# Kernel tuning notes

Measured on AMD Instinct MI355X. Metric: run time of the kernel, lower is better.

Reference implementation:

```python
import jax, jax.numpy as jnp
import numpy as np
import math

D_MODEL = 1024
N_HEADS = 16
D_K = D_MODEL // N_HEADS
D_FF = 4096
B, S = 4, 2048
EPS = 1e-5


def layer_norm(x, scale, bias):
    mu = jnp.mean(x, axis=-1, keepdims=True)
    var = jnp.mean(jnp.square(x - mu), axis=-1, keepdims=True)
    return (x - mu) * jax.lax.rsqrt(var + EPS) * scale + bias


def setup_inputs() -> dict:
    key = jax.random.key(0)
    ks = jax.random.split(key, 16)
    init = lambda k, shape, fan_in: jax.random.normal(k, shape, jnp.float32) / np.sqrt(fan_in)
    x = jax.random.normal(ks[0], (B, S, D_MODEL), jnp.float32)
    # causal mask: positions where mask==0 are blocked
    mask = jnp.tril(jnp.ones((S, S), dtype=bool))[None, None, :, :]
    return {
        "x": x,
        "mask": mask,
        "wq": init(ks[1], (D_MODEL, D_MODEL), D_MODEL), "bq": jnp.zeros((D_MODEL,), jnp.float32),
        "wk": init(ks[2], (D_MODEL, D_MODEL), D_MODEL), "bk": jnp.zeros((D_MODEL,), jnp.float32),
        "wv": init(ks[3], (D_MODEL, D_MODEL), D_MODEL), "bv": jnp.zeros((D_MODEL,), jnp.float32),
        "wo": init(ks[4], (D_MODEL, D_MODEL), D_MODEL), "bo": jnp.zeros((D_MODEL,), jnp.float32),
        "w1": init(ks[5], (D_FF, D_MODEL), D_MODEL), "b1": jnp.zeros((D_FF,), jnp.float32),
        "w2": init(ks[6], (D_MODEL, D_FF), D_FF), "b2": jnp.zeros((D_MODEL,), jnp.float32),
        "ln1_s": jnp.ones((D_MODEL,), jnp.float32), "ln1_b": jnp.zeros((D_MODEL,), jnp.float32),
        "ln2_s": jnp.ones((D_MODEL,), jnp.float32), "ln2_b": jnp.zeros((D_MODEL,), jnp.float32),
    }


def reference(x, mask, wq, bq, wk, bk, wv, bv, wo, bo, w1, b1, w2, b2, ln1_s, ln1_b, ln2_s, ln2_b):
    b, s, _ = x.shape
    # projections (torch Linear: y = x @ W.T + b); split heads -> [b, h, s, d_k]
    def proj(w, bias):
        return (jnp.einsum('bsd,ed->bse', x, w) + bias).reshape(b, s, N_HEADS, D_K).transpose(0, 2, 1, 3)
    Q, K, V = proj(wq, bq), proj(wk, bk), proj(wv, bv)
    scores = jnp.einsum('bhqd,bhkd->bhqk', Q, K) / math.sqrt(D_K)  # [b,h,s,s]
    scores = jnp.where(mask, scores, jnp.float32(-1e9))
    attn = jax.nn.softmax(scores, axis=-1)
    ctx = jnp.einsum('bhqk,bhkd->bhqd', attn, V)
    ctx = ctx.transpose(0, 2, 1, 3).reshape(b, s, D_MODEL)
    attn_out = jnp.einsum('bsd,ed->bse', ctx, wo) + bo
    h = layer_norm(x + attn_out, ln1_s, ln1_b)
    ff = jnp.einsum('bsd,fd->bsf', h, w1) + b1
    ff = jax.nn.gelu(ff, approximate=False)
    ff = jnp.einsum('bsf,df->bsd', ff, w2) + b2
    return layer_norm(h + ff, ln2_s, ln2_b)
```

## Files before the change

kernel.cpp:

```cpp
#include <hip/hip_runtime.h>
#include <hip/hip_bf16.h>
#include <math.h>

using bf16 = __hip_bfloat16;
using bf16x8 = __attribute__((ext_vector_type(8))) short;
using f32x4 = __attribute__((ext_vector_type(4))) float;

#define D_MODEL 1024
#define N_HEADS 16
#define D_K 64
#define D_FF 4096
#define BATCH 4
#define SEQ 2048
#define M_TOT (BATCH*SEQ)

__device__ __forceinline__ void async_copy16(void* lds, const void* g) {
    __builtin_amdgcn_global_load_lds((const __attribute__((address_space(1))) void*)g,
                                     (__attribute__((address_space(3))) void*)lds, 16, 0, 0);
}

__global__ void __launch_bounds__(256) cvt_kernel(const float* __restrict__ src,
                                                  bf16* __restrict__ dst, int n) {
    int nchunk = n >> 2;
    int stride = gridDim.x * blockDim.x;
    for (int i = blockIdx.x * blockDim.x + threadIdx.x; i < nchunk; i += stride) {
        float4 v = *(const float4*)&src[i * 4];
        union { bf16 h[4]; short4 s; } u;
        u.h[0] = __float2bfloat16(v.x);
        u.h[1] = __float2bfloat16(v.y);
        u.h[2] = __float2bfloat16(v.z);
        u.h[3] = __float2bfloat16(v.w);
        *(short4*)&dst[i * 4] = u.s;
    }
}

template<int EPI>
__global__ void __launch_bounds__(256) gemm_bt(const bf16* __restrict__ A,
                                               const bf16* __restrict__ B,
                                               const float* __restrict__ bias,
                                               const float* __restrict__ resid,
                                               float* __restrict__ Cf,
                                               bf16* __restrict__ Cb,
                                               int M, int N, int K) {
    __shared__ __align__(16) bf16 As[128 * 32];
    __shared__ __align__(16) bf16 Bs[128 * 32];
    const int tid  = threadIdx.x;
    const int lane = tid & 63;
    const int wave = tid >> 6;
    const int quad = lane >> 4;
    const int l16  = lane & 15;
    const int wr   = (wave >> 1) * 64;
    const int wc   = (wave & 1) * 64;
    const int m0   = blockIdx.y * 128;
    const int n0   = blockIdx.x * 128;

    const bf16* Ag = A + (size_t)m0 * K;
    const bf16* Bg = B + (size_t)n0 * K;

    f32x4 acc[4][4] = {};

    for (int k0 = 0; k0 < K; k0 += 32) {
        __syncthreads();
#pragma unroll
        for (int p = 0; p < 2; p++) {
            int c = p * 256 + tid;
            int row = c >> 2;
            int col = (c & 3) << 3;
            async_copy16(&As[c * 8], Ag + (size_t)row * K + k0 + col);
            async_copy16(&Bs[c * 8], Bg + (size_t)row * K + k0 + col);
        }
        __syncthreads();
        bf16x8 a[4], b[4];
#pragma unroll
        for (int i = 0; i < 4; i++)
            a[i] = *(const bf16x8*)&As[(wr + i * 16 + l16) * 32 + quad * 8];
#pragma unroll
        for (int j = 0; j < 4; j++)
            b[j] = *(const bf16x8*)&Bs[(wc + j * 16 + l16) * 32 + quad * 8];
#pragma unroll
        for (int i = 0; i < 4; i++)
#pragma unroll
            for (int j = 0; j < 4; j++)
                acc[i][j] = __builtin_amdgcn_mfma_f32_16x16x32_bf16(a[i], b[j], acc[i][j], 0, 0, 0);
    }

#pragma unroll
    for (int i = 0; i < 4; i++) {
#pragma unroll
        for (int r = 0; r < 4; r++) {
            int row = m0 + wr + i * 16 + quad * 4 + r;
            size_t rb = (size_t)row * N;
#pragma unroll
            for (int j = 0; j < 4; j++) {
                int col = n0 + wc + j * 16 + l16;
                float v = acc[i][j][r] + bias[col];
                if (EPI == 0) {
                    Cb[rb + col] = __float2bfloat16(v);
                } else if (EPI == 1) {
                    Cf[rb + col] = v + resid[rb + col];
                } else if (EPI == 2) {
                    float g = 0.5f * v * (1.0f + erff(v * 0.70710678118654752f));
                    Cb[rb + col] = __float2bfloat16(g);
                } else {
                    float sc = (col < 1024) ? 0.18033688011112043f : 1.0f;
                    Cb[rb + col] = __float2bfloat16(v * sc);
                }
            }
        }
    }
}

__global__ void __launch_bounds__(256) attn_kernel(const bf16* __restrict__ qkv,
                                                   bf16* __restrict__ ctx) {
    const int pair = blockIdx.x;
    const int h    = blockIdx.y;
    const int bb   = blockIdx.z;
    const int tid  = threadIdx.x;
    const int lane = tid & 63;
    const int wave = tid >> 6;
    const int quad = lane >> 4;
    const int l16  = lane & 15;

    __shared__ __align__(16) bf16 Pool[4 * 32 * 80];
    __shared__ __align__(16) bf16 Ks[2][64 * 64];
    __shared__ __align__(16) bf16 Vt[2][64 * 80];

    const size_t rowbase = (size_t)(bb * SEQ) * 3072;
    bf16* Pw = &Pool[wave * 32 * 80];
    const int swkey = (l16 >> 2) & 3;

#pragma unroll 1
    for (int phase = 0; phase < 2; phase++) {
        const int qb = (phase == 0) ? pair : (15 - pair);
        const int q0 = qb * 128;
        const int nkb = 2 * (qb + 1);

        __syncthreads();

#pragma unroll
        for (int p = 0; p < 4; p++) {
            int c = p * 256 + tid;
            int row = c >> 3;
            int off = (c & 7) * 8;
            async_copy16(&Pool[c * 8], qkv + rowbase + (size_t)(q0 + row) * 3072 + h * 64 + off);
        }
#pragma unroll
        for (int p = 0; p < 2; p++) {
            int c = p * 256 + tid;
            async_copy16(&Ks[0][c * 8],
                         qkv + rowbase + (size_t)(c >> 3) * 3072 + 1024 + h * 64 + (c & 7) * 8);
        }
        const int vk  = tid & 63;
        const int vd0a = (tid >> 6) * 8;
        const int vd0b = vd0a + 32;
        bf16x8 vr0 = *(const bf16x8*)&qkv[rowbase + (size_t)vk * 3072 + 2048 + h * 64 + vd0a];
        bf16x8 vr1 = *(const bf16x8*)&qkv[rowbase + (size_t)vk * 3072 + 2048 + h * 64 + vd0b];

        __syncthreads();

        bf16x8 aq[2][2];
#pragma unroll
        for (int i = 0; i < 2; i++)
#pragma unroll
            for (int kd = 0; kd < 2; kd++)
                aq[i][kd] = *(const bf16x8*)&Pool[(wave * 32 + i * 16 + l16) * 64 + kd * 32 + quad * 8];

#pragma unroll
        for (int u = 0; u < 8; u++) {
            Vt[0][(vd0a + u) * 80 + vk] = ((const bf16*)&vr0)[u];
            Vt[0][(vd0b + u) * 80 + vk] = ((const bf16*)&vr1)[u];
        }

        f32x4 o[2][4] = {};
        float l_acc[2][4] = {};

#pragma unroll 1
        for (int kb = 0; kb < nkb; kb++) {
            const int cur = kb & 1;
            const int nxt = cur ^ 1;
            __syncthreads();

            const bool pf = (kb + 1 < nkb);
            bf16x8 nv0, nv1;
            if (pf) {
#pragma unroll
                for (int p = 0; p < 2; p++) {
                    int c = p * 256 + tid;
                    async_copy16(&Ks[nxt][c * 8],
                                 qkv + rowbase + (size_t)((kb + 1) * 64 + (c >> 3)) * 3072 + 1024 + h * 64 + (c & 7) * 8);
                }
                nv0 = *(const bf16x8*)&qkv[rowbase + (size_t)((kb + 1) * 64 + vk) * 3072 + 2048 + h * 64 + vd0a];
                nv1 = *(const bf16x8*)&qkv[rowbase + (size_t)((kb + 1) * 64 + vk) * 3072 + 2048 + h * 64 + vd0b];
            }

            f32x4 s[2][4] = {};
#pragma unroll
            for (int jb = 0; jb < 4; jb++) {
#pragma unroll
                for (int kd = 0; kd < 2; kd++) {
                    bf16x8 bk = *(const bf16x8*)&Ks[cur][(jb * 16 + l16) * 64 + kd * 32 + quad * 8];
#pragma unroll
                    for (int i = 0; i < 2; i++)
                        s[i][jb] = __builtin_amdgcn_mfma_f32_16x16x32_bf16(aq[i][kd], bk, s[i][jb], 0, 0, 0);
                }
            }

            if (pf) {
#pragma unroll
                for (int u = 0; u < 8; u++) {
                    Vt[nxt][(vd0a + u) * 80 + vk] = ((const bf16*)&nv0)[u];
                    Vt[nxt][(vd0b + u) * 80 + vk] = ((const bf16*)&nv1)[u];
                }
            }

            const bool diagb = (kb >= 2 * qb);
#pragma unroll
            for (int i = 0; i < 2; i++) {
                const int row0 = q0 + wave * 32 + i * 16;
                const bool needmask = diagb && (kb * 64 + 63 > row0);
#pragma unroll
                for (int jb = 0; jb < 4; jb++) {
                    const int colg = kb * 64 + jb * 16 + l16;
                    const int colsw = ((jb ^ quad) * 16) + l16;
#pragma unroll
                    for (int r = 0; r < 4; r++) {
                        float t = s[i][jb][r];
                        if (needmask && colg > row0 + quad * 4 + r) t = -1e30f;
                        float p = exp2f(t);
                        l_acc[i][r] += p;
                        Pw[(i * 16 + quad * 4 + r) * 80 + colsw] = __float2bfloat16(p);
                    }
                }
            }

#pragma unroll
            for (int kk = 0; kk < 2; kk++) {
                bf16x8 bv[4];
#pragma unroll
                for (int nb = 0; nb < 4; nb++)
                    bv[nb] = *(const bf16x8*)&Vt[cur][(nb * 16 + l16) * 80 + kk * 32 + quad * 8];
                const int grp = kk * 2 + (quad >> 1);
                const int coff = ((grp ^ swkey) * 16) + (quad & 1) * 8;
#pragma unroll
                for (int i = 0; i < 2; i++) {
                    bf16x8 ap = *(const bf16x8*)&Pw[(i * 16 + l16) * 80 + coff];
#pragma unroll
                    for (int nb = 0; nb < 4; nb++)
                        o[i][nb] = __builtin_amdgcn_mfma_f32_16x16x32_bf16(ap, bv[nb], o[i][nb], 0, 0, 0);
                }
            }
        }

#pragma unroll
        for (int i = 0; i < 2; i++)
#pragma unroll
            for (int r = 0; r < 4; r++) {
#pragma unroll
                for (int msk = 1; msk < 16; msk <<= 1)
                    l_acc[i][r] += __shfl_xor(l_acc[i][r], msk, 64);
            }

#pragma unroll
        for (int i = 0; i < 2; i++)
#pragma unroll
            for (int r = 0; r < 4; r++) {
                int rowg = q0 + wave * 32 + i * 16 + quad * 4 + r;
                size_t base = ((size_t)(bb * SEQ + rowg)) * D_MODEL + h * 64;
                float inv = 1.0f / l_acc[i][r];
#pragma unroll
                for (int nb = 0; nb < 4; nb++)
                    ctx[base + nb * 16 + l16] = __float2bfloat16(o[i][nb][r] * inv);
            }
    }
}

__global__ void __launch_bounds__(256) ln_kernel(const float* __restrict__ in,
                                                 const float* __restrict__ sc,
                                                 const float* __restrict__ bi,
                                                 float* __restrict__ of,
                                                 bf16* __restrict__ ob) {
    int row = blockIdx.x;
    const float* rp = in + (size_t)row * D_MODEL;
    int t = threadIdx.x;
    float4 v = *(const float4*)&rp[t * 4];
    float s1 = v.x + v.y + v.z + v.w;
    float s2 = v.x * v.x + v.y * v.y + v.z * v.z + v.w * v.w;
#pragma unroll
    for (int m = 32; m > 0; m >>= 1) {
        s1 += __shfl_xor(s1, m, 64);
        s2 += __shfl_xor(s2, m, 64);
    }
    __shared__ float red[8];
    int wave = t >> 6, lane = t & 63;
    if (lane == 0) { red[wave] = s1; red[wave + 4] = s2; }
    __syncthreads();
    float S1 = red[0] + red[1] + red[2] + red[3];
    float S2 = red[4] + red[5] + red[6] + red[7];
    float mu = S1 * (1.0f / 1024.0f);
    float var = S2 * (1.0f / 1024.0f) - mu * mu;
    float rstd = rsqrtf(var + 1e-5f);
    float4 g = *(const float4*)&sc[t * 4];
    float4 b = *(const float4*)&bi[t * 4];
    float o0 = (v.x - mu) * rstd * g.x + b.x;
    float o1 = (v.y - mu) * rstd * g.y + b.y;
    float o2 = (v.z - mu) * rstd * g.z + b.z;
    float o3 = (v.w - mu) * rstd * g.w + b.w;
    size_t base = (size_t)row * D_MODEL + t * 4;
    if (of) {
        float4 ov; ov.x = o0; ov.y = o1; ov.z = o2; ov.w = o3;
        *(float4*)&of[base] = ov;
    }
    if (ob) {
        union { bf16 h[4]; short4 s; } u;
        u.h[0] = __float2bfloat16(o0);
        u.h[1] = __float2bfloat16(o1);
        u.h[2] = __float2bfloat16(o2);
        u.h[3] = __float2bfloat16(o3);
        *(short4*)&ob[base] = u.s;
    }
}

static const size_t OFF_WQKV = 0;
static const size_t OFF_WO   = 6291456;
static const size_t OFF_W1   = 8388608;
static const size_t OFF_W2   = 16777216;
static const size_t OFF_BQKV = 25165824;
static const size_t OFF_XB   = 25178112;
static const size_t OFF_QKV  = 41955328;
static const size_t OFF_CTX  = 92286976;
static const size_t OFF_HF   = 109064192;
static const size_t OFF_HB   = 142618624;
static const size_t OFF_FF   = 159395840;
static const size_t OFF_RES1 = OFF_QKV;
static const size_t OFF_RES2 = OFF_XB;

extern "C" void kernel_launch(void* const* d_in, const int* in_sizes, int n_in,
                              void* d_out, int out_size, void* d_ws, size_t ws_size,
                              hipStream_t stream) {
    const float* x     = (const float*)d_in[0];
    const float* wq    = (const float*)d_in[2];
    const float* bq    = (const float*)d_in[3];
    const float* wk    = (const float*)d_in[4];
    const float* bk    = (const float*)d_in[5];
    const float* wv    = (const float*)d_in[6];
    const float* bv    = (const float*)d_in[7];
    const float* wo    = (const float*)d_in[8];
    const float* bo    = (const float*)d_in[9];
    const float* w1    = (const float*)d_in[10];
    const float* b1    = (const float*)d_in[11];
    const float* w2    = (const float*)d_in[12];
    const float* b2    = (const float*)d_in[13];
    const float* ln1_s = (const float*)d_in[14];
    const float* ln1_b = (const float*)d_in[15];
    const float* ln2_s = (const float*)d_in[16];
    const float* ln2_b = (const float*)d_in[17];

    char* ws = (char*)d_ws;
    bf16* wqkv_b = (bf16*)(ws + OFF_WQKV);
    bf16* wo_b   = (bf16*)(ws + OFF_WO);
    bf16* w1_b   = (bf16*)(ws + OFF_W1);
    bf16* w2_b   = (bf16*)(ws + OFF_W2);
    float* bqkv  = (float*)(ws + OFF_BQKV);
    bf16* x_b    = (bf16*)(ws + OFF_XB);
    bf16* qkv    = (bf16*)(ws + OFF_QKV);
    bf16* ctx    = (bf16*)(ws + OFF_CTX);
    float* h_f   = (float*)(ws + OFF_HF);
    bf16* h_b    = (bf16*)(ws + OFF_HB);
    bf16* ff     = (bf16*)(ws + OFF_FF);
    float* res1  = (float*)(ws + OFF_RES1);
    float* res2  = (float*)(ws + OFF_RES2);

    cvt_kernel<<<1024, 256, 0, stream>>>(wq, wqkv_b, 1024 * 1024);
    cvt_kernel<<<1024, 256, 0, stream>>>(wk, wqkv_b + 1024 * 1024, 1024 * 1024);
    cvt_kernel<<<1024, 256, 0, stream>>>(wv, wqkv_b + 2 * 1024 * 1024, 1024 * 1024);
    cvt_kernel<<<1024, 256, 0, stream>>>(wo, wo_b, 1024 * 1024);
    cvt_kernel<<<2048, 256, 0, stream>>>(w1, w1_b, 4096 * 1024);
    cvt_kernel<<<2048, 256, 0, stream>>>(w2, w2_b, 4096 * 1024);
    cvt_kernel<<<2048, 256, 0, stream>>>(x, x_b, M_TOT * D_MODEL);
    hipMemcpyAsync(bqkv,        bq, 1024 * sizeof(float), hipMemcpyDeviceToDevice, stream);
    hipMemcpyAsync(bqkv + 1024, bk, 1024 * sizeof(float), hipMemcpyDeviceToDevice, stream);
    hipMemcpyAsync(bqkv + 2048, bv, 1024 * sizeof(float), hipMemcpyDeviceToDevice, stream);

    gemm_bt<3><<<dim3(3072 / 128, M_TOT / 128), 256, 0, stream>>>(
        x_b, wqkv_b, bqkv, nullptr, nullptr, qkv, M_TOT, 3072, 1024);

    attn_kernel<<<dim3(8, N_HEADS, BATCH), 256, 0, stream>>>(qkv, ctx);

    gemm_bt<1><<<dim3(1024 / 128, M_TOT / 128), 256, 0, stream>>>(
        ctx, wo_b, bo, x, res1, nullptr, M_TOT, 1024, 1024);

    ln_kernel<<<M_TOT, 256, 0, stream>>>(res1, ln1_s, ln1_b, h_f, h_b);

    gemm_bt<2><<<dim3(4096 / 128, M_TOT / 128), 256, 0, stream>>>(
        h_b, w1_b, b1, nullptr, nullptr, ff, M_TOT, 4096, 1024);

    gemm_bt<1><<<dim3(1024 / 128, M_TOT / 128), 256, 0, stream>>>(
        ff, w2_b, b2, h_f, res2, nullptr, M_TOT, 1024, 4096);

    ln_kernel<<<M_TOT, 256, 0, stream>>>(res2, ln2_s, ln2_b, (float*)d_out, nullptr);
}
```

Measured before the change: 652.9 us.

## Split-K the FF2 GEMM and fuse partial reduction into final LayerNorm

The second FFN GEMM (K=4096) is split into two K halves that write fp32 partial products to workspace, doubling the block count for better CU fill. A new LayerNorm kernel sums the partials with bias and residual before normalizing, using a one-pass mean/variance. This adds extra fp32 write and read traffic for the partials and uses a simpler single-buffered GEMM loop.

```diff
diff --git a/kernel.cpp b/kernel.cpp
--- a/kernel.cpp
+++ b/kernel.cpp
@@ -110,6 +110,69 @@
     }
 }
 
+__global__ void __launch_bounds__(256) gemm_bt_sk(const bf16* __restrict__ A,
+                                                  const bf16* __restrict__ B,
+                                                  float* __restrict__ P,
+                                                  int M, int N, int K, int KS) {
+    __shared__ __align__(16) bf16 As[128 * 32];
+    __shared__ __align__(16) bf16 Bs[128 * 32];
+    const int tid  = threadIdx.x;
+    const int lane = tid & 63;
+    const int wave = tid >> 6;
+    const int quad = lane >> 4;
+    const int l16  = lane & 15;
+    const int wr   = (wave >> 1) * 64;
+    const int wc   = (wave & 1) * 64;
+    const int m0   = blockIdx.y * 128;
+    const int n0   = blockIdx.x * 128;
+    const int kbeg = blockIdx.z * KS;
+
+    const bf16* Ag = A + (size_t)m0 * K + kbeg;
+    const bf16* Bg = B + (size_t)n0 * K + kbeg;
+    float* Pz = P + (size_t)blockIdx.z * M * N;
+
+    f32x4 acc[4][4] = {};
+
+    for (int k0 = 0; k0 < KS; k0 += 32) {
+        __syncthreads();
+#pragma unroll
+        for (int p = 0; p < 2; p++) {
+            int c = p * 256 + tid;
+            int row = c >> 2;
+            int col = (c & 3) << 3;
+            async_copy16(&As[c * 8], Ag + (size_t)row * K + k0 + col);
+            async_copy16(&Bs[c * 8], Bg + (size_t)row * K + k0 + col);
+        }
+        __syncthreads();
+        bf16x8 a[4], b[4];
+#pragma unroll
+        for (int i = 0; i < 4; i++)
+            a[i] = *(const bf16x8*)&As[(wr + i * 16 + l16) * 32 + quad * 8];
+#pragma unroll
+        for (int j = 0; j < 4; j++)
+            b[j] = *(const bf16x8*)&Bs[(wc + j * 16 + l16) * 32 + quad * 8];
+#pragma unroll
+        for (int i = 0; i < 4; i++)
+#pragma unroll
+            for (int j = 0; j < 4; j++)
+                acc[i][j] = __builtin_amdgcn_mfma_f32_16x16x32_bf16(a[i], b[j], acc[i][j], 0, 0, 0);
+    }
+
+#pragma unroll
+    for (int i = 0; i < 4; i++) {
+#pragma unroll
+        for (int r = 0; r < 4; r++) {
+            int row = m0 + wr + i * 16 + quad * 4 + r;
+            size_t rb = (size_t)row * N;
+#pragma unroll
+            for (int j = 0; j < 4; j++) {
+                int col = n0 + wc + j * 16 + l16;
+                Pz[rb + col] = acc[i][j][r];
+            }
+        }
+    }
+}
+
 __global__ void __launch_bounds__(256) attn_kernel(const bf16* __restrict__ qkv,
                                                    bf16* __restrict__ ctx) {
     const int pair = blockIdx.x;
@@ -320,6 +383,50 @@
     }
 }
 
+__global__ void __launch_bounds__(256) ln2_reduce_kernel(const float* __restrict__ p0,
+                                                         const float* __restrict__ p1,
+                                                         const float* __restrict__ bias,
+                                                         const float* __restrict__ resid,
+                                                         const float* __restrict__ sc,
+                                                         const float* __restrict__ bi,
+                                                         float* __restrict__ out) {
+    int row = blockIdx.x;
+    int t = threadIdx.x;
+    size_t base = (size_t)row * D_MODEL + t * 4;
+    float4 a = *(const float4*)&p0[base];
+    float4 b4 = *(const float4*)&p1[base];
+    float4 rr = *(const float4*)&resid[base];
+    float4 bb = *(const float4*)&bias[t * 4];
+    float v0 = a.x + b4.x + bb.x + rr.x;
+    float v1 = a.y + b4.y + bb.y + rr.y;
+    float v2 = a.z + b4.z + bb.z + rr.z;
+    float v3 = a.w + b4.w + bb.w + rr.w;
+    float s1 = v0 + v1 + v2 + v3;
+    float s2 = v0 * v0 + v1 * v1 + v2 * v2 + v3 * v3;
+#pragma unroll
+    for (int m = 32; m > 0; m >>= 1) {
+        s1 += __shfl_xor(s1, m, 64);
+        s2 += __shfl_xor(s2, m, 64);
+    }
+    __shared__ float red[8];
+    int wave = t >> 6, lane = t & 63;
+    if (lane == 0) { red[wave] = s1; red[wave + 4] = s2; }
+    __syncthreads();
+    float S1 = red[0] + red[1] + red[2] + red[3];
+    float S2 = red[4] + red[5] + red[6] + red[7];
+    float mu = S1 * (1.0f / 1024.0f);
+    float var = S2 * (1.0f / 1024.0f) - mu * mu;
+    float rstd = rsqrtf(var + 1e-5f);
+    float4 g = *(const float4*)&sc[t * 4];
+    float4 bv = *(const float4*)&bi[t * 4];
+    float4 ov;
+    ov.x = (v0 - mu) * rstd * g.x + bv.x;
+    ov.y = (v1 - mu) * rstd * g.y + bv.y;
+    ov.z = (v2 - mu) * rstd * g.z + bv.z;
+    ov.w = (v3 - mu) * rstd * g.w + bv.w;
+    *(float4*)&out[base] = ov;
+}
+
 static const size_t OFF_WQKV = 0;
 static const size_t OFF_WO   = 6291456;
 static const size_t OFF_W1   = 8388608;
@@ -332,7 +439,8 @@
 static const size_t OFF_HB   = 142618624;
 static const size_t OFF_FF   = 159395840;
 static const size_t OFF_RES1 = OFF_QKV;
-static const size_t OFF_RES2 = OFF_XB;
+static const size_t OFF_P0   = OFF_QKV;
+static const size_t OFF_P1   = OFF_QKV + 33554432;
 
 extern "C" void kernel_launch(void* const* d_in, const int* in_sizes, int n_in,
                               void* d_out, int out_size, void* d_ws, size_t ws_size,
@@ -368,7 +476,8 @@
     bf16* h_b    = (bf16*)(ws + OFF_HB);
     bf16* ff     = (bf16*)(ws + OFF_FF);
     float* res1  = (float*)(ws + OFF_RES1);
-    float* res2  = (float*)(ws + OFF_RES2);
+    float* p0    = (float*)(ws + OFF_P0);
+    float* p1    = (float*)(ws + OFF_P1);
 
     cvt_kernel<<<1024, 256, 0, stream>>>(wq, wqkv_b, 1024 * 1024);
     cvt_kernel<<<1024, 256, 0, stream>>>(wk, wqkv_b + 1024 * 1024, 1024 * 1024);
@@ -394,8 +503,8 @@
     gemm_bt<2><<<dim3(4096 / 128, M_TOT / 128), 256, 0, stream>>>(
         h_b, w1_b, b1, nullptr, nullptr, ff, M_TOT, 4096, 1024);
 
-    gemm_bt<1><<<dim3(1024 / 128, M_TOT / 128), 256, 0, stream>>>(
-        ff, w2_b, b2, h_f, res2, nullptr, M_TOT, 1024, 4096);
-
-    ln_kernel<<<M_TOT, 256, 0, stream>>>(res2, ln2_s, ln2_b, (float*)d_out, nullptr);
-}
+    gemm_bt_sk<<<dim3(1024 / 128, M_TOT / 128, 2), 256, 0, stream>>>(
+        ff, w2_b, p0, M_TOT, 1024, 4096, 2048);
+
+    ln2_reduce_kernel<<<M_TOT, 256, 0, stream>>>(p0, p1, b2, h_f, ln2_s, ln2_b, (float*)d_out);
+}
```

Measured after the change: 643.4 us. About the same (-1.5%).
